# Kernel optimization log

Measured on AMD Instinct MI355X. Metric: run time of the kernel, lower is better.

Reference implementation:

```python
import jax, jax.numpy as jnp
import numpy as np

K = 7  # SMorph filter size


def _smorph(x, w, alpha):
    # x: [B,1,H,W]; w: [K,K]; alpha: scalar
    # SMorph(x)(p) = sum_s (x(p+s)+w(s)) * exp(alpha*(x(p+s)+w(s))) / sum_s exp(...)
    patches = jax.lax.conv_general_dilated_patches(
        x, filter_shape=(K, K), window_strides=(1, 1), padding='SAME')  # [B,K*K,H,W]
    z = patches + w.reshape(1, K * K, 1, 1)
    wts = jax.nn.softmax(alpha * z, axis=1)
    out = jnp.sum(z * wts, axis=1, keepdims=True)  # [B,1,H,W]
    return out


def _pool2(x):
    # 2x2 average pool, stride 2; x: [...,H,W]
    B, C, H, W = x.shape
    return x.reshape(B, C, H // 2, 2, W // 2, 2).mean(axis=(3, 5))


def setup_inputs() -> dict:
    key = jax.random.key(0)
    ks = jax.random.split(key, 9)
    B = 512
    return {
        'x': jax.random.normal(ks[0], (B, 1, 28, 28), dtype=jnp.float32),
        'sm_w': 0.5 * jax.random.normal(ks[1], (8, 2, K, K), dtype=jnp.float32),
        'sm_alpha': jax.random.uniform(ks[2], (8, 2), dtype=jnp.float32),
        'W1': jax.random.normal(ks[3], (120, 392), dtype=jnp.float32) / np.sqrt(392),
        'b1': jax.random.normal(ks[4], (120,), dtype=jnp.float32) * 0.01,
        'W2': jax.random.normal(ks[5], (84, 120), dtype=jnp.float32) / np.sqrt(120),
        'b2': jax.random.normal(ks[6], (84,), dtype=jnp.float32) * 0.01,
        'W3': jax.random.normal(ks[7], (10, 84), dtype=jnp.float32) / np.sqrt(84),
        'b3': jax.random.normal(ks[8], (10,), dtype=jnp.float32) * 0.01,
    }


def reference(x, sm_w, sm_alpha, W1, b1, W2, b2, W3, b3):
    B = x.shape[0]

    def branch(w2, a2):
        y = _smorph(x, w2[0], a2[0])
        y = _smorph(y, w2[1], a2[1])
        y = _pool2(_pool2(y))  # [B,1,7,7]
        return y

    ys = jax.vmap(branch)(sm_w, sm_alpha)  # [8,B,1,7,7]
    feat = jnp.transpose(ys, (1, 0, 2, 3, 4)).reshape(B, -1)  # [B,392] = concat(x1..x8)
    h = jax.nn.sigmoid(feat @ W1.T + b1)
    h = jax.nn.sigmoid(h @ W2.T + b2)
    out = jax.nn.sigmoid(h @ W3.T + b3)
    return out
```

## Files before the change

### kernel.cpp

```cpp
#include <hip/hip_runtime.h>

#define HW 28
#define NPIX 784
#define NB 512
#define PR 34
#define PC 52
#define PLANE (PR * PC)

typedef _Float16 half8 __attribute__((ext_vector_type(8)));
typedef float    f32x4 __attribute__((ext_vector_type(4)));

union H8 { unsigned short s[8]; uint2 u2[2]; half8 h; };

__device__ __forceinline__ void mconv(const _Float16 (*ev)[PC],
                                      const _Float16 (*pv)[PC],
                                      const unsigned short (*tbl)[7][48],
                                      int q, int n15, f32x4 o[2][2])
{
    f32x4 num[2][2], den[2][2];
#pragma unroll
    for (int a = 0; a < 2; ++a)
#pragma unroll
        for (int c = 0; c < 2; ++c) {
            num[a][c] = (f32x4){0.f, 0.f, 0.f, 0.f};
            den[a][c] = (f32x4){0.f, 0.f, 0.f, 0.f};
        }

    const int bp = 16 + 4 * q - n15;

#pragma unroll
    for (int di = 0; di < 7; ++di) {
        H8 bq, be;
        const unsigned short* tq = &tbl[0][di][0];
        const unsigned short* te = &tbl[1][di][0];
#pragma unroll
        for (int j = 0; j < 4; ++j) {
            bq.s[j]     = tq[bp + j];
            bq.s[4 + j] = tq[bp + 16 + j];
            be.s[j]     = te[bp + j];
            be.s[4 + j] = te[bp + 16 + j];
        }
#pragma unroll
        for (int rt = 0; rt < 2; ++rt) {
            const int row = rt * 12 + di + n15;
#pragma unroll
            for (int ct = 0; ct < 2; ++ct) {
                const int col = ct * 16 + 4 * q;
                H8 ea, pa;
                ea.u2[0] = *(const uint2*)&ev[row][col];
                ea.u2[1] = *(const uint2*)&ev[row][col + 16];
                pa.u2[0] = *(const uint2*)&pv[row][col];
                pa.u2[1] = *(const uint2*)&pv[row][col + 16];
                num[rt][ct] = __builtin_amdgcn_mfma_f32_16x16x32_f16(ea.h, bq.h, num[rt][ct], 0, 0, 0);
                num[rt][ct] = __builtin_amdgcn_mfma_f32_16x16x32_f16(pa.h, be.h, num[rt][ct], 0, 0, 0);
                den[rt][ct] = __builtin_amdgcn_mfma_f32_16x16x32_f16(ea.h, be.h, den[rt][ct], 0, 0, 0);
            }
        }
    }
#pragma unroll
    for (int a = 0; a < 2; ++a)
#pragma unroll
        for (int c = 0; c < 2; ++c)
#pragma unroll
            for (int v = 0; v < 4; ++v)
                o[a][c][v] = num[a][c][v] * __builtin_amdgcn_rcpf(den[a][c][v]);
}

__device__ __forceinline__ float sigmoidf_(float s) {
    return __builtin_amdgcn_rcpf(1.f + __expf(-s));
}

__global__ __launch_bounds__(512, 2) void smorph_net_kernel(
    const float* __restrict__ x,
    const float* __restrict__ sw,
    const float* __restrict__ sa,
    const float* __restrict__ W1, const float* __restrict__ b1,
    const float* __restrict__ W2, const float* __restrict__ b2,
    const float* __restrict__ W3, const float* __restrict__ b3,
    float* __restrict__ out)
{
    __shared__ __align__(16) _Float16       planes[8][2][PR][PC];
    __shared__ __align__(16) unsigned short wtbl[8][2][7][48];
    __shared__ __align__(16) float          mlp[392 + 120 + 128];

    const int b    = blockIdx.x;
    const int tid  = threadIdx.x;
    const int f    = tid >> 6;
    const int lane = tid & 63;
    const int n15  = lane & 15;
    const int q    = lane >> 4;

    _Float16 (*ev)[PC] = planes[f][0];
    _Float16 (*pv)[PC] = planes[f][1];
    const float* src = x + (size_t)b * NPIX;

    const float a1 = sa[f * 2 + 0];
    const float a2 = sa[f * 2 + 1];

    unsigned wp1 = 0, wp2 = 0;
    if (lane < 49) {
        union { _Float16 h[2]; unsigned u; } p;
        float w1v = sw[(f * 2 + 0) * 49 + lane];
        float e1  = __expf(a1 * w1v);
        p.h[0] = (_Float16)(w1v * e1);
        p.h[1] = (_Float16)e1;
        wp1 = p.u;
        float w2v = sw[(f * 2 + 1) * 49 + lane];
        float e2  = __expf(a2 * w2v);
        p.h[0] = (_Float16)(w2v * e2);
        p.h[1] = (_Float16)e2;
        wp2 = p.u;
    }

    {
        unsigned* tz = (unsigned*)&wtbl[f][0][0][0];
        for (int i = lane; i < 336; i += 64) tz[i] = 0;
    }
    if (lane < 49) {
        int di = lane / 7, t = lane - di * 7;
        wtbl[f][0][di][16 + t] = (unsigned short)(wp1 & 0xFFFF);
        wtbl[f][1][di][16 + t] = (unsigned short)(wp1 >> 16);
    }

    {
        unsigned* evu = (unsigned*)&planes[f][0][0][0];
        unsigned* pvu = (unsigned*)&planes[f][1][0][0];
        for (int i = lane; i < PLANE / 2; i += 64) {
            evu[i] = 0x3C003C00u;
            pvu[i] = 0u;
        }
    }

#pragma unroll
    for (int k = 0; k < 13; ++k) {
        int p = lane + 64 * k;
        if (p < NPIX) {
            float v = src[p];
            int pi = p / HW;
            int pj = p - pi * HW;
            float e = __expf(a1 * v);
            ev[pi + 3][pj + 3] = (_Float16)e;
            pv[pi + 3][pj + 3] = (_Float16)(v * e);
        }
    }

    f32x4 o1_[2][2];
    mconv(ev, pv, wtbl[f], q, n15, o1_);

#pragma unroll
    for (int rt = 0; rt < 2; ++rt)
#pragma unroll
        for (int ct = 0; ct < 2; ++ct) {
            if (ct == 1 && n15 >= 12) continue;
#pragma unroll
            for (int v = 0; v < 4; ++v) {
                int row = rt * 12 + 4 * q + v;
                int col = ct * 16 + n15;
                float ov = o1_[rt][ct][v];
                float e  = __expf(a2 * ov);
                ev[row + 3][col + 3] = (_Float16)e;
                pv[row + 3][col + 3] = (_Float16)(ov * e);
            }
        }

    if (lane < 49) {
        int di = lane / 7, t = lane - di * 7;
        wtbl[f][0][di][16 + t] = (unsigned short)(wp2 & 0xFFFF);
        wtbl[f][1][di][16 + t] = (unsigned short)(wp2 >> 16);
    }

    f32x4 o2_[2][2];
    mconv(ev, pv, wtbl[f], q, n15, o2_);

    float* feat = mlp;
    float* h1   = mlp + 392;
    float* h2   = mlp + 512;

#pragma unroll
    for (int rt = 0; rt < 2; ++rt)
#pragma unroll
        for (int ct = 0; ct < 2; ++ct) {
            float s = o2_[rt][ct][0] + o2_[rt][ct][1] + o2_[rt][ct][2] + o2_[rt][ct][3];
            s += __shfl_xor(s, 1);
            s += __shfl_xor(s, 2);
            int pr = rt ? (3 + q) : q;
            int pc = (ct ? 4 : 0) + (n15 >> 2);
            bool ok = ((n15 & 3) == 0)
                   && !(rt == 1 && q == 0)
                   && !(ct == 1 && n15 >= 12);
            if (ok) feat[f * 49 + pr * 7 + pc] = s * 0.0625f;
        }
    __syncthreads();

    if (tid < 480) {
        int n = tid >> 2, h = tid & 3;
        const float4* wr = (const float4*)(W1 + n * 392);
        const float4* fv = (const float4*)feat;
        float c0 = 0.f, c1 = 0.f, c2 = 0.f, c3 = 0.f;
#pragma unroll 2
        for (int k = h; k < 98; k += 4) {
            float4 w = wr[k];
            float4 v = fv[k];
            c0 = fmaf(w.x, v.x, c0);
            c1 = fmaf(w.y, v.y, c1);
            c2 = fmaf(w.z, v.z, c2);
            c3 = fmaf(w.w, v.w, c3);
        }
        float acc = (c0 + c1) + (c2 + c3);
        acc += __shfl_xor(acc, 1);
        acc += __shfl_xor(acc, 2);
        if (h == 0) h1[n] = sigmoidf_(acc + b1[n]);
    }
    __syncthreads();

    if (tid < 336) {
        int n = tid >> 2, h = tid & 3;
        const float4* wr = (const float4*)(W2 + n * 120);
        const float4* hv = (const float4*)h1;
        float c0 = 0.f, c1 = 0.f, c2 = 0.f, c3 = 0.f;
        for (int k = h; k < 30; k += 4) {
            float4 w = wr[k];
            float4 v = hv[k];
            c0 = fmaf(w.x, v.x, c0);
            c1 = fmaf(w.y, v.y, c1);
            c2 = fmaf(w.z, v.z, c2);
            c3 = fmaf(w.w, v.w, c3);
        }
        float acc = (c0 + c1) + (c2 + c3);
        acc += __shfl_xor(acc, 1);
        acc += __shfl_xor(acc, 2);
        if (h == 0) h2[n] = sigmoidf_(acc + b2[n]);
    }
    __syncthreads();

    if (tid < 40) {
        int n = tid >> 2, qh = tid & 3;
        const float4* wr = (const float4*)(W3 + n * 84);
        const float4* hv = (const float4*)h2;
        float c0 = 0.f, c1 = 0.f, c2 = 0.f, c3 = 0.f;
        for (int k = qh; k < 21; k += 4) {
            float4 w = wr[k];
            float4 v = hv[k];
            c0 = fmaf(w.x, v.x, c0);
            c1 = fmaf(w.y, v.y, c1);
            c2 = fmaf(w.z, v.z, c2);
            c3 = fmaf(w.w, v.w, c3);
        }
        float acc = (c0 + c1) + (c2 + c3);
        acc += __shfl_xor(acc, 1);
        acc += __shfl_xor(acc, 2);
        if (qh == 0) out[(size_t)b * 10 + n] = sigmoidf_(acc + b3[n]);
    }
}

extern "C" void kernel_launch(void* const* d_in, const int* in_sizes, int n_in,
                              void* d_out, int out_size, void* d_ws, size_t ws_size,
                              hipStream_t stream) {
    const float* x  = (const float*)d_in[0];
    const float* sw = (const float*)d_in[1];
    const float* sa = (const float*)d_in[2];
    const float* W1 = (const float*)d_in[3];
    const float* b1 = (const float*)d_in[4];
    const float* W2 = (const float*)d_in[5];
    const float* b2 = (const float*)d_in[6];
    const float* W3 = (const float*)d_in[7];
    const float* b3 = (const float*)d_in[8];
    float* out = (float*)d_out;

    smorph_net_kernel<<<NB, 512, 0, stream>>>(x, sw, sa, W1, b1, W2, b2, W3, b3, out);
}
```

Measured before the change: 106.4 us.

## Process two images per block to share weight tables and MLP weight loads

```diff
diff --git a/kernel.cpp b/kernel.cpp
--- a/kernel.cpp
+++ b/kernel.cpp
@@ -2,7 +2,8 @@
 
 #define HW 28
 #define NPIX 784
-#define NB 512
+#define NIMG 512
+#define NBLK 256
 #define PR 34
 #define PC 52
 #define PLANE (PR * PC)
@@ -12,19 +13,21 @@
 
 union H8 { unsigned short s[8]; uint2 u2[2]; half8 h; };
 
-__device__ __forceinline__ void mconv(const _Float16 (*ev)[PC],
-                                      const _Float16 (*pv)[PC],
-                                      const unsigned short (*tbl)[7][48],
-                                      int q, int n15, f32x4 o[2][2])
+__device__ __forceinline__ void mconv2(const _Float16 (*ev0)[PC], const _Float16 (*pv0)[PC],
+                                       const _Float16 (*ev1)[PC], const _Float16 (*pv1)[PC],
+                                       const unsigned short (*tbl)[7][48],
+                                       int q, int n15, f32x4 o[2][2][2])
 {
-    f32x4 num[2][2], den[2][2];
-#pragma unroll
-    for (int a = 0; a < 2; ++a)
-#pragma unroll
-        for (int c = 0; c < 2; ++c) {
-            num[a][c] = (f32x4){0.f, 0.f, 0.f, 0.f};
-            den[a][c] = (f32x4){0.f, 0.f, 0.f, 0.f};
-        }
+    f32x4 num[2][2][2], den[2][2][2];
+#pragma unroll
+    for (int i = 0; i < 2; ++i)
+#pragma unroll
+        for (int a = 0; a < 2; ++a)
+#pragma unroll
+            for (int c = 0; c < 2; ++c) {
+                num[i][a][c] = (f32x4){0.f, 0.f, 0.f, 0.f};
+                den[i][a][c] = (f32x4){0.f, 0.f, 0.f, 0.f};
+            }
 
     const int bp = 16 + 4 * q - n15;
 
@@ -46,31 +49,40 @@
 #pragma unroll
             for (int ct = 0; ct < 2; ++ct) {
                 const int col = ct * 16 + 4 * q;
-                H8 ea, pa;
-                ea.u2[0] = *(const uint2*)&ev[row][col];
-                ea.u2[1] = *(const uint2*)&ev[row][col + 16];
-                pa.u2[0] = *(const uint2*)&pv[row][col];
-                pa.u2[1] = *(const uint2*)&pv[row][col + 16];
-                num[rt][ct] = __builtin_amdgcn_mfma_f32_16x16x32_f16(ea.h, bq.h, num[rt][ct], 0, 0, 0);
-                num[rt][ct] = __builtin_amdgcn_mfma_f32_16x16x32_f16(pa.h, be.h, num[rt][ct], 0, 0, 0);
-                den[rt][ct] = __builtin_amdgcn_mfma_f32_16x16x32_f16(ea.h, be.h, den[rt][ct], 0, 0, 0);
+                H8 ea0, pa0, ea1, pa1;
+                ea0.u2[0] = *(const uint2*)&ev0[row][col];
+                ea0.u2[1] = *(const uint2*)&ev0[row][col + 16];
+                pa0.u2[0] = *(const uint2*)&pv0[row][col];
+                pa0.u2[1] = *(const uint2*)&pv0[row][col + 16];
+                ea1.u2[0] = *(const uint2*)&ev1[row][col];
+                ea1.u2[1] = *(const uint2*)&ev1[row][col + 16];
+                pa1.u2[0] = *(const uint2*)&pv1[row][col];
+                pa1.u2[1] = *(const uint2*)&pv1[row][col + 16];
+                num[0][rt][ct] = __builtin_amdgcn_mfma_f32_16x16x32_f16(ea0.h, bq.h, num[0][rt][ct], 0, 0, 0);
+                num[1][rt][ct] = __builtin_amdgcn_mfma_f32_16x16x32_f16(ea1.h, bq.h, num[1][rt][ct], 0, 0, 0);
+                num[0][rt][ct] = __builtin_amdgcn_mfma_f32_16x16x32_f16(pa0.h, be.h, num[0][rt][ct], 0, 0, 0);
+                num[1][rt][ct] = __builtin_amdgcn_mfma_f32_16x16x32_f16(pa1.h, be.h, num[1][rt][ct], 0, 0, 0);
+                den[0][rt][ct] = __builtin_amdgcn_mfma_f32_16x16x32_f16(ea0.h, be.h, den[0][rt][ct], 0, 0, 0);
+                den[1][rt][ct] = __builtin_amdgcn_mfma_f32_16x16x32_f16(ea1.h, be.h, den[1][rt][ct], 0, 0, 0);
             }
         }
     }
 #pragma unroll
-    for (int a = 0; a < 2; ++a)
-#pragma unroll
-        for (int c = 0; c < 2; ++c)
-#pragma unroll
-            for (int v = 0; v < 4; ++v)
-                o[a][c][v] = num[a][c][v] * __builtin_amdgcn_rcpf(den[a][c][v]);
+    for (int i = 0; i < 2; ++i)
+#pragma unroll
+        for (int a = 0; a < 2; ++a)
+#pragma unroll
+            for (int c = 0; c < 2; ++c)
+#pragma unroll
+                for (int v = 0; v < 4; ++v)
+                    o[i][a][c][v] = num[i][a][c][v] * __builtin_amdgcn_rcpf(den[i][a][c][v]);
 }
 
 __device__ __forceinline__ float sigmoidf_(float s) {
     return __builtin_amdgcn_rcpf(1.f + __expf(-s));
 }
 
-__global__ __launch_bounds__(512, 2) void smorph_net_kernel(
+__global__ __launch_bounds__(512, 1) void smorph_net_kernel(
     const float* __restrict__ x,
     const float* __restrict__ sw,
     const float* __restrict__ sa,
@@ -79,20 +91,23 @@
     const float* __restrict__ W3, const float* __restrict__ b3,
     float* __restrict__ out)
 {
-    __shared__ __align__(16) _Float16       planes[8][2][PR][PC];
+    __shared__ __align__(16) _Float16       planes[8][2][2][PR][PC];
     __shared__ __align__(16) unsigned short wtbl[8][2][7][48];
-    __shared__ __align__(16) float          mlp[392 + 120 + 128];
-
-    const int b    = blockIdx.x;
+    __shared__ __align__(16) float          mlp2[2][640];
+
+    const int b0   = blockIdx.x * 2;
     const int tid  = threadIdx.x;
     const int f    = tid >> 6;
     const int lane = tid & 63;
     const int n15  = lane & 15;
     const int q    = lane >> 4;
 
-    _Float16 (*ev)[PC] = planes[f][0];
-    _Float16 (*pv)[PC] = planes[f][1];
-    const float* src = x + (size_t)b * NPIX;
+    _Float16 (*ev0)[PC] = planes[f][0][0];
+    _Float16 (*pv0)[PC] = planes[f][0][1];
+    _Float16 (*ev1)[PC] = planes[f][1][0];
+    _Float16 (*pv1)[PC] = planes[f][1][1];
+    const float* src0 = x + (size_t)b0 * NPIX;
+    const float* src1 = src0 + NPIX;
 
     const float a1 = sa[f * 2 + 0];
     const float a2 = sa[f * 2 + 1];
@@ -123,11 +138,13 @@
     }
 
     {
-        unsigned* evu = (unsigned*)&planes[f][0][0][0];
-        unsigned* pvu = (unsigned*)&planes[f][1][0][0];
+        unsigned* e0u = (unsigned*)&planes[f][0][0][0][0];
+        unsigned* p0u = (unsigned*)&planes[f][0][1][0][0];
+        unsigned* e1u = (unsigned*)&planes[f][1][0][0][0];
+        unsigned* p1u = (unsigned*)&planes[f][1][1][0][0];
         for (int i = lane; i < PLANE / 2; i += 64) {
-            evu[i] = 0x3C003C00u;
-            pvu[i] = 0u;
+            e0u[i] = 0x3C003C00u; p0u[i] = 0u;
+            e1u[i] = 0x3C003C00u; p1u[i] = 0u;
         }
     }
 
@@ -135,17 +152,21 @@
     for (int k = 0; k < 13; ++k) {
         int p = lane + 64 * k;
         if (p < NPIX) {
-            float v = src[p];
+            float v0 = src0[p];
+            float v1 = src1[p];
             int pi = p / HW;
             int pj = p - pi * HW;
-            float e = __expf(a1 * v);
-            ev[pi + 3][pj + 3] = (_Float16)e;
-            pv[pi + 3][pj + 3] = (_Float16)(v * e);
-        }
-    }
-
-    f32x4 o1_[2][2];
-    mconv(ev, pv, wtbl[f], q, n15, o1_);
+            float e0 = __expf(a1 * v0);
+            float e1 = __expf(a1 * v1);
+            ev0[pi + 3][pj + 3] = (_Float16)e0;
+            pv0[pi + 3][pj + 3] = (_Float16)(v0 * e0);
+            ev1[pi + 3][pj + 3] = (_Float16)e1;
+            pv1[pi + 3][pj + 3] = (_Float16)(v1 * e1);
+        }
+    }
+
+    f32x4 o1_[2][2][2];
+    mconv2(ev0, pv0, ev1, pv1, wtbl[f], q, n15, o1_);
 
 #pragma unroll
     for (int rt = 0; rt < 2; ++rt)
@@ -156,10 +177,14 @@
             for (int v = 0; v < 4; ++v) {
                 int row = rt * 12 + 4 * q + v;
                 int col = ct * 16 + n15;
-                float ov = o1_[rt][ct][v];
-                float e  = __expf(a2 * ov);
-                ev[row + 3][col + 3] = (_Float16)e;
-                pv[row + 3][col + 3] = (_Float16)(ov * e);
+                float ova = o1_[0][rt][ct][v];
+                float ovb = o1_[1][rt][ct][v];
+                float ea  = __expf(a2 * ova);
+                float eb  = __expf(a2 * ovb);
+                ev0[row + 3][col + 3] = (_Float16)ea;
+                pv0[row + 3][col + 3] = (_Float16)(ova * ea);
+                ev1[row + 3][col + 3] = (_Float16)eb;
+                pv1[row + 3][col + 3] = (_Float16)(ovb * eb);
             }
         }
 
@@ -169,87 +194,113 @@
         wtbl[f][1][di][16 + t] = (unsigned short)(wp2 >> 16);
     }
 
-    f32x4 o2_[2][2];
-    mconv(ev, pv, wtbl[f], q, n15, o2_);
-
-    float* feat = mlp;
-    float* h1   = mlp + 392;
-    float* h2   = mlp + 512;
+    f32x4 o2_[2][2][2];
+    mconv2(ev0, pv0, ev1, pv1, wtbl[f], q, n15, o2_);
+
+    float* feat0 = mlp2[0];
+    float* feat1 = mlp2[1];
 
 #pragma unroll
     for (int rt = 0; rt < 2; ++rt)
 #pragma unroll
         for (int ct = 0; ct < 2; ++ct) {
-            float s = o2_[rt][ct][0] + o2_[rt][ct][1] + o2_[rt][ct][2] + o2_[rt][ct][3];
-            s += __shfl_xor(s, 1);
-            s += __shfl_xor(s, 2);
+            float s0 = o2_[0][rt][ct][0] + o2_[0][rt][ct][1] + o2_[0][rt][ct][2] + o2_[0][rt][ct][3];
+            float s1 = o2_[1][rt][ct][0] + o2_[1][rt][ct][1] + o2_[1][rt][ct][2] + o2_[1][rt][ct][3];
+            s0 += __shfl_xor(s0, 1);  s1 += __shfl_xor(s1, 1);
+            s0 += __shfl_xor(s0, 2);  s1 += __shfl_xor(s1, 2);
             int pr = rt ? (3 + q) : q;
             int pc = (ct ? 4 : 0) + (n15 >> 2);
             bool ok = ((n15 & 3) == 0)
                    && !(rt == 1 && q == 0)
                    && !(ct == 1 && n15 >= 12);
-            if (ok) feat[f * 49 + pr * 7 + pc] = s * 0.0625f;
+            if (ok) {
+                feat0[f * 49 + pr * 7 + pc] = s0 * 0.0625f;
+                feat1[f * 49 + pr * 7 + pc] = s1 * 0.0625f;
+            }
         }
     __syncthreads();
+
+    float* h1_0 = mlp2[0] + 392;  float* h2_0 = mlp2[0] + 512;
+    float* h1_1 = mlp2[1] + 392;  float* h2_1 = mlp2[1] + 512;
 
     if (tid < 480) {
         int n = tid >> 2, h = tid & 3;
         const float4* wr = (const float4*)(W1 + n * 392);
-        const float4* fv = (const float4*)feat;
-        float c0 = 0.f, c1 = 0.f, c2 = 0.f, c3 = 0.f;
-#pragma unroll 2
+        const float4* f0 = (const float4*)feat0;
+        const float4* f1 = (const float4*)feat1;
+        float a00 = 0.f, a01 = 0.f, a02 = 0.f, a03 = 0.f;
+        float a10 = 0.f, a11 = 0.f, a12 = 0.f, a13 = 0.f;
         for (int k = h; k < 98; k += 4) {
-            float4 w = wr[k];
-            float4 v = fv[k];
-            c0 = fmaf(w.x, v.x, c0);
-            c1 = fmaf(w.y, v.y, c1);
-            c2 = fmaf(w.z, v.z, c2);
-            c3 = fmaf(w.w, v.w, c3);
-        }
-        float acc = (c0 + c1) + (c2 + c3);
-        acc += __shfl_xor(acc, 1);
-        acc += __shfl_xor(acc, 2);
-        if (h == 0) h1[n] = sigmoidf_(acc + b1[n]);
+            float4 w  = wr[k];
+            float4 u0 = f0[k];
+            float4 u1 = f1[k];
+            a00 = fmaf(w.x, u0.x, a00);  a10 = fmaf(w.x, u1.x, a10);
+            a01 = fmaf(w.y, u0.y, a01);  a11 = fmaf(w.y, u1.y, a11);
+            a02 = fmaf(w.z, u0.z, a02);  a12 = fmaf(w.z, u1.z, a12);
+            a03 = fmaf(w.w, u0.w, a03);  a13 = fmaf(w.w, u1.w, a13);
+        }
+        float acc0 = (a00 + a01) + (a02 + a03);
+        float acc1 = (a10 + a11) + (a12 + a13);
+        acc0 += __shfl_xor(acc0, 1);  acc1 += __shfl_xor(acc1, 1);
+        acc0 += __shfl_xor(acc0, 2);  acc1 += __shfl_xor(acc1, 2);
+        if (h == 0) {
+            h1_0[n] = sigmoidf_(acc0 + b1[n]);
+            h1_1[n] = sigmoidf_(acc1 + b1[n]);
+        }
     }
     __syncthreads();
 
     if (tid < 336) {
         int n = tid >> 2, h = tid & 3;
         const float4* wr = (const float4*)(W2 + n * 120);
-        const float4* hv = (const float4*)h1;
-        float c0 = 0.f, c1 = 0.f, c2 = 0.f, c3 = 0.f;
+        const float4* v0 = (const float4*)h1_0;
+        const float4* v1 = (const float4*)h1_1;
+        float a00 = 0.f, a01 = 0.f, a02 = 0.f, a03 = 0.f;
+        float a10 = 0.f, a11 = 0.f, a12 = 0.f, a13 = 0.f;
         for (int k = h; k < 30; k += 4) {
-            float4 w = wr[k];
-            float4 v = hv[k];
-            c0 = fmaf(w.x, v.x, c0);
-            c1 = fmaf(w.y, v.y, c1);
-            c2 = fmaf(w.z, v.z, c2);
-            c3 = fmaf(w.w, v.w, c3);
-        }
-        float acc = (c0 + c1) + (c2 + c3);
-        acc += __shfl_xor(acc, 1);
-        acc += __shfl_xor(acc, 2);
-        if (h == 0) h2[n] = sigmoidf_(acc + b2[n]);
+            float4 w  = wr[k];
+            float4 u0 = v0[k];
+            float4 u1 = v1[k];
+            a00 = fmaf(w.x, u0.x, a00);  a10 = fmaf(w.x, u1.x, a10);
+            a01 = fmaf(w.y, u0.y, a01);  a11 = fmaf(w.y, u1.y, a11);
+            a02 = fmaf(w.z, u0.z, a02);  a12 = fmaf(w.z, u1.z, a12);
+            a03 = fmaf(w.w, u0.w, a03);  a13 = fmaf(w.w, u1.w, a13);
+        }
+        float acc0 = (a00 + a01) + (a02 + a03);
+        float acc1 = (a10 + a11) + (a12 + a13);
+        acc0 += __shfl_xor(acc0, 1);  acc1 += __shfl_xor(acc1, 1);
+        acc0 += __shfl_xor(acc0, 2);  acc1 += __shfl_xor(acc1, 2);
+        if (h == 0) {
+            h2_0[n] = sigmoidf_(acc0 + b2[n]);
+            h2_1[n] = sigmoidf_(acc1 + b2[n]);
+        }
     }
     __syncthreads();
 
     if (tid < 40) {
         int n = tid >> 2, qh = tid & 3;
         const float4* wr = (const float4*)(W3 + n * 84);
-        const float4* hv = (const float4*)h2;
-        float c0 = 0.f, c1 = 0.f, c2 = 0.f, c3 = 0.f;
+        const float4* v0 = (const float4*)h2_0;
+        const float4* v1 = (const float4*)h2_1;
+        float a00 = 0.f, a01 = 0.f, a02 = 0.f, a03 = 0.f;
+        float a10 = 0.f, a11 = 0.f, a12 = 0.f, a13 = 0.f;
         for (int k = qh; k < 21; k += 4) {
-            float4 w = wr[k];
-            float4 v = hv[k];
-            c0 = fmaf(w.x, v.x, c0);
-            c1 = fmaf(w.y, v.y, c1);
-            c2 = fmaf(w.z, v.z, c2);
-            c3 = fmaf(w.w, v.w, c3);
-        }
-        float acc = (c0 + c1) + (c2 + c3);
-        acc += __shfl_xor(acc, 1);
-        acc += __shfl_xor(acc, 2);
-        if (qh == 0) out[(size_t)b * 10 + n] = sigmoidf_(acc + b3[n]);
+            float4 w  = wr[k];
+            float4 u0 = v0[k];
+            float4 u1 = v1[k];
+            a00 = fmaf(w.x, u0.x, a00);  a10 = fmaf(w.x, u1.x, a10);
+            a01 = fmaf(w.y, u0.y, a01);  a11 = fmaf(w.y, u1.y, a11);
+            a02 = fmaf(w.z, u0.z, a02);  a12 = fmaf(w.z, u1.z, a12);
+            a03 = fmaf(w.w, u0.w, a03);  a13 = fmaf(w.w, u1.w, a13);
+        }
+        float acc0 = (a00 + a01) + (a02 + a03);
+        float acc1 = (a10 + a11) + (a12 + a13);
+        acc0 += __shfl_xor(acc0, 1);  acc1 += __shfl_xor(acc1, 1);
+        acc0 += __shfl_xor(acc0, 2);  acc1 += __shfl_xor(acc1, 2);
+        if (qh == 0) {
+            out[(size_t)b0 * 10 + n]       = sigmoidf_(acc0 + b3[n]);
+            out[(size_t)(b0 + 1) * 10 + n] = sigmoidf_(acc1 + b3[n]);
+        }
     }
 }
 
@@ -267,5 +318,5 @@
     const float* b3 = (const float*)d_in[8];
     float* out = (float*)d_out;
 
-    smorph_net_kernel<<<NB, 512, 0, stream>>>(x, sw, sa, W1, b1, W2, b2, W3, b3, out);
+    smorph_net_kernel<<<NBLK, 512, 0, stream>>>(x, sw, sa, W1, b1, W2, b2, W3, b3, out);
 }
```

Result: faster. 102.1 us (-4.0%).
